# Kernel tuning notes

Hardware: AMD Instinct MI355X
Metric: run time of the kernel (lower is better)

## Reference

```python
import jax, jax.numpy as jnp
import numpy as np

CONTEXT = 32
NUM_EMB = 128
HEAD_SIZE = 64


def setup_inputs() -> dict:
    key = jax.random.key(0)
    kx, kk, kq, kv = jax.random.split(key, 4)
    B, T, C, H = 16384, CONTEXT, NUM_EMB, HEAD_SIZE
    # weights stored as [C, H] so projection is x @ W (equiv to torch Linear(C,H,bias=False))
    s = 1.0 / np.sqrt(C)
    return {
        "x": jax.random.normal(kx, (B, T, C), dtype=jnp.float32),
        "Wk": jax.random.uniform(kk, (C, H), jnp.float32, -s, s),
        "Wq": jax.random.uniform(kq, (C, H), jnp.float32, -s, s),
        "Wv": jax.random.uniform(kv, (C, H), jnp.float32, -s, s),
    }


def reference(x, Wk, Wq, Wv):
    B, T, C = x.shape
    H = Wk.shape[1]
    k = x @ Wk  # [B, T, H]
    q = x @ Wq  # [B, T, H]
    v = x @ Wv  # [B, T, H]
    scale = H ** (-0.5)
    wei = jnp.einsum("bth,bsh->bts", q, k) * scale  # [B, T, T]
    causal = jnp.tril(jnp.ones((T, T), dtype=bool))
    wei = jnp.where(causal, wei, -jnp.inf)
    wei = jax.nn.softmax(wei, axis=-1)
    return jnp.einsum("bts,bsh->bth", wei, v)  # [B, T, H]
```

## Files before the change

kernel.cpp:

```cpp
#include <hip/hip_runtime.h>
#include <stdint.h>
#include <math.h>

#define T_CTX 32
#define C_EMB 128
#define H_DIM 64
#define NB    8
#define WROW  136

typedef __bf16 bf16x8 __attribute__((ext_vector_type(8)));
typedef float  f32x16 __attribute__((ext_vector_type(16)));

union Frag {
  uint32_t w[4];
  bf16x8   v;
};
static_assert(sizeof(Frag) == 16, "frag size");

__device__ __forceinline__ uint32_t cvt_pk(float a, float b) {
  uint32_t r;
  asm("v_cvt_pk_bf16_f32 %0, %1, %2" : "=v"(r) : "v"(a), "v"(b));
  return r;
}
__device__ __forceinline__ void swap32(uint32_t &a, uint32_t &b) {
  asm("v_permlane32_swap_b32 %0, %1" : "+v"(a), "+v"(b));
}
__device__ __forceinline__ float bf_lo_f(uint32_t w) {
  union { uint32_t u; float f; } c; c.u = w << 16; return c.f;
}
__device__ __forceinline__ float bf_hi_f(uint32_t w) {
  union { uint32_t u; float f; } c; c.u = w & 0xffff0000u; return c.f;
}

__device__ __forceinline__ f32x16 mfma(const Frag &a, const Frag &b, const f32x16 &c) {
  return __builtin_amdgcn_mfma_f32_32x32x16_bf16(a.v, b.v, c, 0, 0, 0);
}

__device__ __forceinline__ void cvt8(const float4 &a, const float4 &b, Frag &h, Frag &l) {
  float f[8] = {a.x, a.y, a.z, a.w, b.x, b.y, b.z, b.w};
#pragma unroll
  for (int j = 0; j < 4; ++j) {
    uint32_t hw = cvt_pk(f[2 * j], f[2 * j + 1]);
    float r0 = f[2 * j]     - bf_lo_f(hw);
    float r1 = f[2 * j + 1] - bf_hi_f(hw);
    h.w[j] = hw;
    l.w[j] = cvt_pk(r0, r1);
  }
}

__device__ __forceinline__ void make2(const float *a, Frag &f0, Frag &f1) {
  uint32_t x, y;
  x = cvt_pk(a[0], a[1]);   y = cvt_pk(a[4], a[5]);   swap32(x, y); f0.w[0] = x; f0.w[2] = y;
  x = cvt_pk(a[2], a[3]);   y = cvt_pk(a[6], a[7]);   swap32(x, y); f0.w[1] = x; f0.w[3] = y;
  x = cvt_pk(a[8], a[9]);   y = cvt_pk(a[12], a[13]); swap32(x, y); f1.w[0] = x; f1.w[2] = y;
  x = cvt_pk(a[10], a[11]); y = cvt_pk(a[14], a[15]); swap32(x, y); f1.w[1] = x; f1.w[3] = y;
}

__global__ __launch_bounds__(256) void head_fused(
    const float* __restrict__ x, const float* __restrict__ Wk,
    const float* __restrict__ Wq, const float* __restrict__ Wv,
    float* __restrict__ out, int nbatch) {
  __shared__ unsigned short wt[3 * H_DIM * WROW];

  const int tid = threadIdx.x;
  {
    const float* Ws[3] = {Wq, Wk, Wv};
#pragma unroll
    for (int wi = 0; wi < 3; ++wi) {
      const float* W = Ws[wi];
#pragma unroll
      for (int it = 0; it < 8; ++it) {
        int e = (it * 256 + tid) * 4;
        float4 f = *(const float4*)(W + e);
        int c = e >> 6, h = e & 63;
        uint32_t w01 = cvt_pk(f.x, f.y);
        uint32_t w23 = cvt_pk(f.z, f.w);
        unsigned short* bp = &wt[(wi * H_DIM + h) * WROW + c];
        bp[0 * WROW] = (unsigned short)(w01 & 0xffffu);
        bp[1 * WROW] = (unsigned short)(w01 >> 16);
        bp[2 * WROW] = (unsigned short)(w23 & 0xffffu);
        bp[3 * WROW] = (unsigned short)(w23 >> 16);
      }
    }
  }
  __syncthreads();

  const int wave = tid >> 6, lane = tid & 63;
  const int col = lane & 31, hi = lane >> 5;

  const unsigned short* wq0 = &wt[(0 * H_DIM + col) * WROW + hi * 8];
  const unsigned short* wq1 = wq0 + 32 * WROW;
  const unsigned short* wk0 = wq0 + 64 * WROW;
  const unsigned short* wk1 = wq0 + 96 * WROW;
  const unsigned short* wv0 = wq0 + 128 * WROW;
  const unsigned short* wv1 = wq0 + 160 * WROW;

  for (int it = 0; it < NB; ++it) {
    int batch = blockIdx.x * (4 * NB) + it * 4 + wave;
    if (batch >= nbatch) break;
    const float* xp = x + (size_t)batch * (T_CTX * C_EMB) + col * C_EMB + hi * 8;

    Frag xh[8], xl[8];
#pragma unroll
    for (int kk = 0; kk < 8; ++kk) {
      float4 a = *(const float4*)(xp + kk * 16);
      float4 b = *(const float4*)(xp + kk * 16 + 4);
      cvt8(a, b, xh[kk], xl[kk]);
    }

    f32x16 q0{}, q1{};
#pragma unroll
    for (int kk = 0; kk < 8; ++kk) {
      Frag w0, w1;
      w0.v = *(const bf16x8*)(wq0 + kk * 16);
      w1.v = *(const bf16x8*)(wq1 + kk * 16);
      q0 = mfma(w0, xh[kk], q0); q0 = mfma(w0, xl[kk], q0);
      q1 = mfma(w1, xh[kk], q1); q1 = mfma(w1, xl[kk], q1);
    }
    Frag qf[4];
    { float t[16];
#pragma unroll
      for (int r = 0; r < 16; ++r) t[r] = q0[r];
      make2(t, qf[0], qf[1]);
#pragma unroll
      for (int r = 0; r < 16; ++r) t[r] = q1[r];
      make2(t, qf[2], qf[3]);
    }

    f32x16 k0{}, k1{};
#pragma unroll
    for (int kk = 0; kk < 8; ++kk) {
      Frag w0, w1;
      w0.v = *(const bf16x8*)(wk0 + kk * 16);
      w1.v = *(const bf16x8*)(wk1 + kk * 16);
      k0 = mfma(w0, xh[kk], k0); k0 = mfma(w0, xl[kk], k0);
      k1 = mfma(w1, xh[kk], k1); k1 = mfma(w1, xl[kk], k1);
    }
    Frag kf[4];
    { float t[16];
#pragma unroll
      for (int r = 0; r < 16; ++r) t[r] = k0[r];
      make2(t, kf[0], kf[1]);
#pragma unroll
      for (int r = 0; r < 16; ++r) t[r] = k1[r];
      make2(t, kf[2], kf[3]);
    }

    f32x16 va{}, vb{};
#pragma unroll
    for (int kk = 0; kk < 8; ++kk) {
      Frag w0, w1;
      w0.v = *(const bf16x8*)(wv0 + kk * 16);
      w1.v = *(const bf16x8*)(wv1 + kk * 16);
      va = mfma(xh[kk], w0, va); va = mfma(xl[kk], w0, va);
      vb = mfma(xh[kk], w1, vb); vb = mfma(xl[kk], w1, vb);
    }

    f32x16 st{};
#pragma unroll
    for (int ks = 0; ks < 4; ++ks) st = mfma(kf[ks], qf[ks], st);

    float p[16];
    float m = -INFINITY;
#pragma unroll
    for (int r = 0; r < 16; ++r) {
      int key = (r & 3) + 8 * (r >> 2) + 4 * hi;
      float sv = st[r] * 0.125f;
      p[r] = (key > col) ? -INFINITY : sv;
      m = fmaxf(m, p[r]);
    }
    m = fmaxf(m, __shfl_xor(m, 32));
    float sum = 0.f;
#pragma unroll
    for (int r = 0; r < 16; ++r) {
      p[r] = exp2f((p[r] - m) * 1.4426950408889634f);
      sum += p[r];
    }
    sum += __shfl_xor(sum, 32);
    float inv = 1.0f / sum;
#pragma unroll
    for (int r = 0; r < 16; ++r) p[r] *= inv;

    Frag pa0, pa1;
    make2(p, pa0, pa1);

    Frag vfa0, vfa1, vfb0, vfb1;
    { float t[16];
#pragma unroll
      for (int r = 0; r < 16; ++r) t[r] = va[r];
      make2(t, vfa0, vfa1);
#pragma unroll
      for (int r = 0; r < 16; ++r) t[r] = vb[r];
      make2(t, vfb0, vfb1);
    }

    f32x16 o0{}, o1{};
    o0 = mfma(pa0, vfa0, o0); o0 = mfma(pa1, vfa1, o0);
    o1 = mfma(pa0, vfb0, o1); o1 = mfma(pa1, vfb1, o1);

    float* op = out + (size_t)batch * (T_CTX * H_DIM) + col;
#pragma unroll
    for (int r = 0; r < 16; ++r) {
      int trow = (r & 3) + 8 * (r >> 2) + 4 * hi;
      op[trow * H_DIM]      = o0[r];
      op[trow * H_DIM + 32] = o1[r];
    }
  }
}

extern "C" void kernel_launch(void* const* d_in, const int* in_sizes, int n_in,
                              void* d_out, int out_size, void* d_ws, size_t ws_size,
                              hipStream_t stream) {
  (void)n_in; (void)out_size; (void)d_ws; (void)ws_size;
  const float* x  = (const float*)d_in[0];
  const float* Wk = (const float*)d_in[1];
  const float* Wq = (const float*)d_in[2];
  const float* Wv = (const float*)d_in[3];
  float* out = (float*)d_out;
  int B = in_sizes[0] / (T_CTX * C_EMB);
  int grid = (B + 4 * NB - 1) / (4 * NB);
  head_fused<<<dim3(grid), dim3(256), 0, stream>>>(x, Wk, Wq, Wv, out, B);
}
```

Before: 95.29 us.

## Fuse QKV projection loops, vectorize output stores, raise occupancy

Merges the three separate Q/K/V projection loops into one loop that converts each x chunk to hi/lo bf16 on the fly, so the 16 x fragments no longer have to stay live in registers. Adds a launch-bounds minimum of 3 blocks per CU and cuts batches per block from 8 to 2, giving more blocks and better occupancy. Swaps the operand order of the final PV MFMA so each lane holds contiguous output columns and can write float4 stores instead of scalar strided stores. Smaller NB means the weight conversion into shared memory is repeated by more blocks, and the register cap may cause spills.

```diff
diff --git a/kernel.cpp b/kernel.cpp
--- a/kernel.cpp
+++ b/kernel.cpp
@@ -5,7 +5,7 @@
 #define T_CTX 32
 #define C_EMB 128
 #define H_DIM 64
-#define NB    8
+#define NB    2
 #define WROW  136
 
 typedef __bf16 bf16x8 __attribute__((ext_vector_type(8)));
@@ -56,7 +56,7 @@
   x = cvt_pk(a[10], a[11]); y = cvt_pk(a[14], a[15]); swap32(x, y); f1.w[1] = x; f1.w[3] = y;
 }
 
-__global__ __launch_bounds__(256) void head_fused(
+__global__ __launch_bounds__(256, 3) void head_fused(
     const float* __restrict__ x, const float* __restrict__ Wk,
     const float* __restrict__ Wq, const float* __restrict__ Wv,
     float* __restrict__ out, int nbatch) {
@@ -88,36 +88,36 @@
   const int wave = tid >> 6, lane = tid & 63;
   const int col = lane & 31, hi = lane >> 5;
 
-  const unsigned short* wq0 = &wt[(0 * H_DIM + col) * WROW + hi * 8];
-  const unsigned short* wq1 = wq0 + 32 * WROW;
-  const unsigned short* wk0 = wq0 + 64 * WROW;
-  const unsigned short* wk1 = wq0 + 96 * WROW;
-  const unsigned short* wv0 = wq0 + 128 * WROW;
-  const unsigned short* wv1 = wq0 + 160 * WROW;
+  const unsigned short* wb = &wt[col * WROW + hi * 8];
 
   for (int it = 0; it < NB; ++it) {
     int batch = blockIdx.x * (4 * NB) + it * 4 + wave;
     if (batch >= nbatch) break;
     const float* xp = x + (size_t)batch * (T_CTX * C_EMB) + col * C_EMB + hi * 8;
 
-    Frag xh[8], xl[8];
+    f32x16 q0{}, q1{}, k0{}, k1{}, va{}, vb{};
 #pragma unroll
     for (int kk = 0; kk < 8; ++kk) {
       float4 a = *(const float4*)(xp + kk * 16);
       float4 b = *(const float4*)(xp + kk * 16 + 4);
-      cvt8(a, b, xh[kk], xl[kk]);
-    }
-
-    f32x16 q0{}, q1{};
-#pragma unroll
-    for (int kk = 0; kk < 8; ++kk) {
-      Frag w0, w1;
-      w0.v = *(const bf16x8*)(wq0 + kk * 16);
-      w1.v = *(const bf16x8*)(wq1 + kk * 16);
-      q0 = mfma(w0, xh[kk], q0); q0 = mfma(w0, xl[kk], q0);
-      q1 = mfma(w1, xh[kk], q1); q1 = mfma(w1, xl[kk], q1);
-    }
-    Frag qf[4];
+      Frag xh, xl;
+      cvt8(a, b, xh, xl);
+      Frag f0, f1;
+      f0.v = *(const bf16x8*)(wb + (0 * 32) * WROW + kk * 16);
+      f1.v = *(const bf16x8*)(wb + (1 * 32) * WROW + kk * 16);
+      q0 = mfma(f0, xh, q0); q0 = mfma(f0, xl, q0);
+      q1 = mfma(f1, xh, q1); q1 = mfma(f1, xl, q1);
+      f0.v = *(const bf16x8*)(wb + (2 * 32) * WROW + kk * 16);
+      f1.v = *(const bf16x8*)(wb + (3 * 32) * WROW + kk * 16);
+      k0 = mfma(f0, xh, k0); k0 = mfma(f0, xl, k0);
+      k1 = mfma(f1, xh, k1); k1 = mfma(f1, xl, k1);
+      f0.v = *(const bf16x8*)(wb + (4 * 32) * WROW + kk * 16);
+      f1.v = *(const bf16x8*)(wb + (5 * 32) * WROW + kk * 16);
+      va = mfma(xh, f0, va); va = mfma(xl, f0, va);
+      vb = mfma(xh, f1, vb); vb = mfma(xl, f1, vb);
+    }
+
+    Frag qf[4], kf[4];
     { float t[16];
 #pragma unroll
       for (int r = 0; r < 16; ++r) t[r] = q0[r];
@@ -125,35 +125,12 @@
 #pragma unroll
       for (int r = 0; r < 16; ++r) t[r] = q1[r];
       make2(t, qf[2], qf[3]);
-    }
-
-    f32x16 k0{}, k1{};
-#pragma unroll
-    for (int kk = 0; kk < 8; ++kk) {
-      Frag w0, w1;
-      w0.v = *(const bf16x8*)(wk0 + kk * 16);
-      w1.v = *(const bf16x8*)(wk1 + kk * 16);
-      k0 = mfma(w0, xh[kk], k0); k0 = mfma(w0, xl[kk], k0);
-      k1 = mfma(w1, xh[kk], k1); k1 = mfma(w1, xl[kk], k1);
-    }
-    Frag kf[4];
-    { float t[16];
 #pragma unroll
       for (int r = 0; r < 16; ++r) t[r] = k0[r];
       make2(t, kf[0], kf[1]);
 #pragma unroll
       for (int r = 0; r < 16; ++r) t[r] = k1[r];
       make2(t, kf[2], kf[3]);
-    }
-
-    f32x16 va{}, vb{};
-#pragma unroll
-    for (int kk = 0; kk < 8; ++kk) {
-      Frag w0, w1;
-      w0.v = *(const bf16x8*)(wv0 + kk * 16);
-      w1.v = *(const bf16x8*)(wv1 + kk * 16);
-      va = mfma(xh[kk], w0, va); va = mfma(xl[kk], w0, va);
-      vb = mfma(xh[kk], w1, vb); vb = mfma(xl[kk], w1, vb);
     }
 
     f32x16 st{};
@@ -195,15 +172,16 @@
     }
 
     f32x16 o0{}, o1{};
-    o0 = mfma(pa0, vfa0, o0); o0 = mfma(pa1, vfa1, o0);
-    o1 = mfma(pa0, vfb0, o1); o1 = mfma(pa1, vfb1, o1);
-
-    float* op = out + (size_t)batch * (T_CTX * H_DIM) + col;
-#pragma unroll
-    for (int r = 0; r < 16; ++r) {
-      int trow = (r & 3) + 8 * (r >> 2) + 4 * hi;
-      op[trow * H_DIM]      = o0[r];
-      op[trow * H_DIM + 32] = o1[r];
+    o0 = mfma(vfa0, pa0, o0); o0 = mfma(vfa1, pa1, o0);
+    o1 = mfma(vfb0, pa0, o1); o1 = mfma(vfb1, pa1, o1);
+
+    float* op = out + (size_t)batch * (T_CTX * H_DIM) + col * H_DIM + 4 * hi;
+#pragma unroll
+    for (int b = 0; b < 4; ++b) {
+      float4 s0 = {o0[4 * b], o0[4 * b + 1], o0[4 * b + 2], o0[4 * b + 3]};
+      float4 s1 = {o1[4 * b], o1[4 * b + 1], o1[4 * b + 2], o1[4 * b + 3]};
+      *(float4*)(op + 8 * b)      = s0;
+      *(float4*)(op + 32 + 8 * b) = s1;
     }
   }
 }
```

After: 118.5 us. +24.3%, slower.
